# Performance work log

Hardware: AMD Instinct MI355X
Metric: run time of the kernel (lower is better)

Reference implementation:

```python
import jax, jax.numpy as jnp
import numpy as np

TEMPERATURE = 0.07
EPS = 1e-6  # arccosh domain clamp: argument must be >= 1


def setup_inputs() -> dict:
    key = jax.random.key(0)
    k1, k2 = jax.random.split(key)
    N, D = 8192, 768
    v_hyp = jax.random.normal(k1, (N, D), dtype=jnp.float32)
    t_hyp = jax.random.normal(k2, (N, D), dtype=jnp.float32)
    c = jnp.float32(1.0)  # curvature (positive scalar)
    return {"v_hyp": v_hyp, "t_hyp": t_hyp, "c": c}


def _pairwise_hyperbolic_dist(v, t, c):
    # Lorentz/hyperboloid pairwise distance with curvature c:
    #   x_time = sqrt(1/c + ||x||^2)
    #   <x,y>_L = x . y - x_time * y_time
    #   d(x,y) = (1/sqrt(c)) * arccosh(clamp(-c * <x,y>_L, min=1+eps))
    inv_c = 1.0 / c
    v_time = jnp.sqrt(inv_c + jnp.sum(v * v, axis=-1))  # [N]
    t_time = jnp.sqrt(inv_c + jnp.sum(t * t, axis=-1))  # [N]
    lorentz = jnp.einsum("nd,md->nm", v, t) - v_time[:, None] * t_time[None, :]
    arg = jnp.maximum(-c * lorentz, 1.0 + EPS)
    return jnp.sqrt(inv_c) * jnp.arccosh(arg)  # [N, N]


def _ce_diag(logits):
    # cross-entropy with labels = arange(N), mean reduction
    logp = jax.nn.log_softmax(logits, axis=-1)
    return -jnp.mean(jnp.diagonal(logp))


def reference(v_hyp, t_hyp, c):
    dist = _pairwise_hyperbolic_dist(v_hyp, t_hyp, c)
    logits = -dist / TEMPERATURE  # [N, N]
    loss_v2t = _ce_diag(logits)
    loss_t2v = _ce_diag(logits.T)
    return (loss_v2t + loss_t2v) * 0.5
```

## Files before the change

### kernel.cpp

```cpp
#include <hip/hip_runtime.h>
#include <hip/hip_bf16.h>
#include <math.h>

#define NROWS 8192
#define DDIM  768
#define TEMP_INV 14.285714285714286f
#define EPSX 1e-6f
#define NKT  12
#define SHIFT 55.0f
#define SHIFT_E 79.34282475f
#define QS   20.0f
#define SLOT 16384

typedef __attribute__((ext_vector_type(4))) int   i32x4;
typedef unsigned int   u32;

#define GLOAD16(gaddr, laddr)                                                   \
  __builtin_amdgcn_global_load_lds(                                             \
      (const __attribute__((address_space(1))) u32*)(gaddr),                    \
      (__attribute__((address_space(3))) u32*)(laddr), 16, 0, 0)

#define MFMAI8(a,b,c) __builtin_amdgcn_mfma_i32_16x16x64_i8((a),(b),(c),0,0,0)

__device__ __forceinline__ u32 q8(float x){
  int q = __float2int_rn(x * QS);
  q = q < -127 ? -127 : (q > 127 ? 127 : q);
  return (u32)(q & 255);
}

template<int CTRL>
__device__ __forceinline__ float dpp_rot_add(float v){
  int r = __builtin_amdgcn_update_dpp(0, __float_as_int(v), CTRL, 0xF, 0xF, true);
  return v + __int_as_float(r);
}
__device__ __forceinline__ float row_sum16(float v){
  v = dpp_rot_add<0x121>(v);
  v = dpp_rot_add<0x122>(v);
  v = dpp_rot_add<0x124>(v);
  v = dpp_rot_add<0x128>(v);
  return v;
}

__global__ __launch_bounds__(256) void prep_kernel(
    const float* __restrict__ v, const float* __restrict__ t, const float* __restrict__ cptr,
    u32* __restrict__ vb, u32* __restrict__ tb,
    float* __restrict__ vtime, float* __restrict__ ttime, float* __restrict__ diag)
{
  const int row  = blockIdx.x * 4 + (threadIdx.x >> 6);
  const int lane = threadIdx.x & 63;
  const float inv_c = 1.0f / cptr[0];
  const float4* vr = (const float4*)(v + (size_t)row * DDIM);
  const float4* tr = (const float4*)(t + (size_t)row * DDIM);
  u32* vbr = vb + (size_t)row * (DDIM/4);
  u32* tbr = tb + (size_t)row * (DDIM/4);
  float sv = 0.f, st = 0.f, dd = 0.f;
  #pragma unroll
  for (int it = 0; it < 3; it++){
    int k = lane + it*64;
    float4 a = vr[k], b = tr[k];
    sv += a.x*a.x + a.y*a.y + a.z*a.z + a.w*a.w;
    st += b.x*b.x + b.y*b.y + b.z*b.z + b.w*b.w;
    dd += a.x*b.x + a.y*b.y + a.z*b.z + a.w*b.w;
    vbr[k] = q8(a.x) | (q8(a.y)<<8) | (q8(a.z)<<16) | (q8(a.w)<<24);
    tbr[k] = q8(b.x) | (q8(b.y)<<8) | (q8(b.z)<<16) | (q8(b.w)<<24);
  }
  #pragma unroll
  for (int o = 32; o; o >>= 1){
    sv += __shfl_down(sv, o);
    st += __shfl_down(st, o);
    dd += __shfl_down(dd, o);
  }
  if (!lane){
    vtime[row] = sqrtf(inv_c + sv);
    ttime[row] = sqrtf(inv_c + st);
    diag[row]  = dd;
  }
}

__global__ __launch_bounds__(512, 6) void tile_kernel(
    const char* __restrict__ vb, const char* __restrict__ tb,
    const float* __restrict__ vtime, const float* __restrict__ ttime,
    const float* __restrict__ cptr,
    float* __restrict__ rowPsum, float* __restrict__ colPsum)
{
  __shared__ char SMc[3*SLOT];
  __shared__ float vtl2[128], ttl[128];

  const int tid = threadIdx.x;
  const int lane = tid & 63, wid = tid >> 6;
  const int wm = wid >> 1, wn = wid & 1;
  const int lo = lane & 15, hi = lane >> 4;

  const float c = cptr[0];
  const float c2 = c + c;
  const float slog = -(1.0f/sqrtf(c)) * TEMP_INV;
  const float wmin = c2 * (1.0f + EPSX);
  const float kq   = c2 * (1.0f/(QS*QS));

  const int linear = blockIdx.x;
  const int xcd = linear & 7, s = linear >> 3;
  const int xr = xcd & 1, xc = xcd >> 1;
  const int by = xr*32 + (s & 3) + ((s >> 6) << 2);
  const int bx = xc*16 + ((s >> 2) & 15);

  if (tid < 128){ vtl2[tid] = c2 * vtime[by*128 + tid]; }
  else if (tid < 256){ ttl[tid-128] = ttime[bx*128 + tid - 128]; }

  const char* Abase = vb + (size_t)(by*128) * DDIM;
  const char* Bbase = tb + (size_t)(bx*128) * DDIM;

  const int sx = (tid >> 3) & 3;
  const char* pA = Abase + (size_t)(tid >> 2)*DDIM + ((tid & 3) ^ sx)*16;
  const char* pB = Bbase + (size_t)(tid >> 2)*DDIM + ((tid & 3) ^ sx)*16;
  const int dA = wid*1024;
  const int dB = 8192 + wid*1024;

  const int swb  = (hi ^ ((lo >> 1) & 3)) * 16;
  const int arow = (wm*32 + lo) * 64 + swb;
  const int brow = 8192 + (wn*64 + lo) * 64 + swb;

  i32x4 acc[2][4];
  #pragma unroll
  for (int m = 0; m < 2; m++)
    #pragma unroll
    for (int n = 0; n < 4; n++)
      acc[m][n] = (i32x4){0,0,0,0};

#define STG(kt) do{                                                              \
    char* s_ = SMc + ((kt) % 3) * SLOT;                                          \
    GLOAD16(pA + (kt)*64, s_ + dA);                                              \
    GLOAD16(pB + (kt)*64, s_ + dB); }while(0)

  STG(0); STG(1);
  asm volatile("s_waitcnt vmcnt(2) lgkmcnt(0)" ::: "memory");
  __builtin_amdgcn_s_barrier();

  #pragma unroll
  for (int t = 0; t < NKT; t++){
    __builtin_amdgcn_sched_barrier(0);
    const char* S = SMc + (t % 3) * SLOT;
    if (t + 2 < NKT) STG(t + 2);
    i32x4 b[4];
    #pragma unroll
    for (int n = 0; n < 4; n++) b[n] = *(const i32x4*)(S + brow + n*1024);
    i32x4 a0 = *(const i32x4*)(S + arow);
    i32x4 a1 = *(const i32x4*)(S + arow + 1024);
    __builtin_amdgcn_s_setprio(1);
    #pragma unroll
    for (int n = 0; n < 4; n++){
      acc[0][n] = MFMAI8(a0, b[n], acc[0][n]);
      acc[1][n] = MFMAI8(a1, b[n], acc[1][n]);
    }
    __builtin_amdgcn_s_setprio(0);
    if (t < NKT-2)       asm volatile("s_waitcnt vmcnt(2) lgkmcnt(0)" ::: "memory");
    else if (t == NKT-2) asm volatile("s_waitcnt vmcnt(0) lgkmcnt(0)" ::: "memory");
    else                 asm volatile("s_waitcnt lgkmcnt(0)" ::: "memory");
    __builtin_amdgcn_s_barrier();
  }
#undef STG

  __syncthreads();

  #pragma unroll
  for (int m = 0; m < 2; m++){
    #pragma unroll
    for (int n = 0; n < 4; n++){
      #pragma unroll
      for (int q = 0; q < 4; q++){
        int r  = wm*32 + m*16 + hi*4 + q;
        int cc = wn*64 + n*16 + lo;
        float w = fmaf(-kq, (float)acc[m][n][q], vtl2[r] * ttl[cc]);
        w = fmaxf(w, wmin);
        acc[m][n][q] = __float_as_int(exp2f(fmaf(slog, log2f(w), SHIFT_E)));
      }
    }
  }

  float* reds  = (float*)SMc;
  float* redcs = reds + 256;

  #pragma unroll
  for (int m = 0; m < 2; m++){
    #pragma unroll
    for (int q = 0; q < 4; q++){
      float s2 = (__int_as_float(acc[m][0][q]) + __int_as_float(acc[m][1][q]))
               + (__int_as_float(acc[m][2][q]) + __int_as_float(acc[m][3][q]));
      s2 = row_sum16(s2);
      if (lo == 0)
        reds[wn*128 + wm*32 + m*16 + hi*4 + q] = s2;
    }
  }
  __syncthreads();
  if (tid < 128){
    float S = reds[tid] + reds[128 + tid];
    rowPsum[(size_t)bx*NROWS + by*128 + tid] = S;
  }

  #pragma unroll
  for (int n = 0; n < 4; n++){
    float s2 = 0.f;
    #pragma unroll
    for (int m = 0; m < 2; m++)
      #pragma unroll
      for (int q = 0; q < 4; q++) s2 += __int_as_float(acc[m][n][q]);
    s2 += __shfl_xor(s2, 16);
    s2 += __shfl_xor(s2, 32);
    if (hi == 0)
      redcs[wm*128 + wn*64 + n*16 + lo] = s2;
  }
  __syncthreads();
  if (tid < 128){
    float S = (redcs[tid] + redcs[128 + tid]) + (redcs[256 + tid] + redcs[384 + tid]);
    colPsum[(size_t)by*NROWS + bx*128 + tid] = S;
  }
}

__global__ __launch_bounds__(256) void lse_reduce(
    const float* __restrict__ rowPsum, const float* __restrict__ colPsum,
    float* __restrict__ psums)
{
  const int i = blockIdx.x * 256 + threadIdx.x;
  const float* Ps = blockIdx.y ? colPsum : rowPsum;
  float S = 0.f;
  for (int b = 0; b < 64; b++)
    S += Ps[(size_t)b*NROWS + i];
  float lse = __logf(S) - SHIFT;
  for (int o = 32; o; o >>= 1) lse += __shfl_down(lse, o);
  __shared__ float red[4];
  int lane = threadIdx.x & 63, wid = threadIdx.x >> 6;
  if (!lane) red[wid] = lse;
  __syncthreads();
  if (!threadIdx.x)
    psums[blockIdx.y*32 + blockIdx.x] = red[0]+red[1]+red[2]+red[3];
}

__global__ __launch_bounds__(1024) void final_kernel(
    const float* __restrict__ psums, const float* __restrict__ vtime,
    const float* __restrict__ ttime, const float* __restrict__ diag,
    const float* __restrict__ cptr, float* __restrict__ out)
{
  int tid = threadIdx.x;
  float c = cptr[0];
  float slog = -(1.0f/sqrtf(c)) * TEMP_INV;
  float dsum = 0.f;
  #pragma unroll
  for (int it = 0; it < 8; it++){
    int i = tid + it*1024;
    float arg = c * (vtime[i]*ttime[i] - diag[i]);
    arg = fmaxf(arg, 1.0f + EPSX);
    dsum += slog * __logf(arg + sqrtf(arg*arg - 1.0f));
  }
  for (int o = 32; o; o >>= 1) dsum += __shfl_down(dsum, o);
  __shared__ float red[16];
  if (!(tid & 63)) red[tid >> 6] = dsum;
  __syncthreads();
  if (tid < 64){
    float p = psums[tid];
    for (int o = 32; o; o >>= 1) p += __shfl_down(p, o);
    if (!tid){
      float dtot = 0.f;
      #pragma unroll
      for (int k = 0; k < 16; k++) dtot += red[k];
      out[0] = 0.5f*p/NROWS - dtot/NROWS;
    }
  }
}

extern "C" void kernel_launch(void* const* d_in, const int* in_sizes, int n_in,
                              void* d_out, int out_size, void* d_ws, size_t ws_size,
                              hipStream_t stream) {
  const float* v = (const float*)d_in[0];
  const float* t = (const float*)d_in[1];
  const float* c = (const float*)d_in[2];

  char* ws = (char*)d_ws;
  const size_t NB = (size_t)NROWS * DDIM;
  char*  vb      = ws;
  char*  tb      = ws + NB;
  float* vtime   = (float*)(ws + 2*NB);
  float* ttime   = (float*)(ws + 2*NB + NROWS*4);
  float* diag    = (float*)(ws + 2*NB + 2*(size_t)NROWS*4);
  char*  p       = ws + 2*NB + 3*(size_t)NROWS*4;
  float* rowPsum = (float*)(p);
  float* colPsum = (float*)(p + (size_t)64*NROWS*4);
  float* psums   = (float*)(p + (size_t)128*NROWS*4);

  prep_kernel<<<2048, 256, 0, stream>>>(v, t, c, (u32*)vb, (u32*)tb, vtime, ttime, diag);
  tile_kernel<<<4096, 512, 0, stream>>>(vb, tb, vtime, ttime, c, rowPsum, colPsum);
  lse_reduce<<<dim3(32, 2), 256, 0, stream>>>(rowPsum, colPsum, psums);
  final_kernel<<<1, 1024, 0, stream>>>(psums, vtime, ttime, diag, c, (float*)d_out);
}
```

Baseline: 101.4 us.

## Store quantized int8 operands in k-tile planar pre-swizzled layout

The prep kernel now writes the int8-quantized v and t matrices as 12 k-tile planes, each holding 64 bytes per row, with the LDS bank swizzle already applied. The tile kernel's async global-to-LDS loads therefore read one contiguous 1 KB chunk per wave per stage instead of 64-byte pieces strided by the row length. This should improve global-load coalescing and simplify address math in the GEMM loop. In exchange, the prep kernel uses only 48 of 64 lanes and writes 16-byte stores scattered across planes.

```diff
diff --git a/kernel.cpp b/kernel.cpp
--- a/kernel.cpp
+++ b/kernel.cpp
@@ -11,6 +11,7 @@
 #define SHIFT_E 79.34282475f
 #define QS   20.0f
 #define SLOT 16384
+#define PLANE ((size_t)NROWS * 64)
 
 typedef __attribute__((ext_vector_type(4))) int   i32x4;
 typedef unsigned int   u32;
@@ -43,7 +44,7 @@
 
 __global__ __launch_bounds__(256) void prep_kernel(
     const float* __restrict__ v, const float* __restrict__ t, const float* __restrict__ cptr,
-    u32* __restrict__ vb, u32* __restrict__ tb,
+    char* __restrict__ vp, char* __restrict__ tp,
     float* __restrict__ vtime, float* __restrict__ ttime, float* __restrict__ diag)
 {
   const int row  = blockIdx.x * 4 + (threadIdx.x >> 6);
@@ -51,18 +52,28 @@
   const float inv_c = 1.0f / cptr[0];
   const float4* vr = (const float4*)(v + (size_t)row * DDIM);
   const float4* tr = (const float4*)(t + (size_t)row * DDIM);
-  u32* vbr = vb + (size_t)row * (DDIM/4);
-  u32* tbr = tb + (size_t)row * (DDIM/4);
   float sv = 0.f, st = 0.f, dd = 0.f;
-  #pragma unroll
-  for (int it = 0; it < 3; it++){
-    int k = lane + it*64;
-    float4 a = vr[k], b = tr[k];
-    sv += a.x*a.x + a.y*a.y + a.z*a.z + a.w*a.w;
-    st += b.x*b.x + b.y*b.y + b.z*b.z + b.w*b.w;
-    dd += a.x*b.x + a.y*b.y + a.z*b.z + a.w*b.w;
-    vbr[k] = q8(a.x) | (q8(a.y)<<8) | (q8(a.z)<<16) | (q8(a.w)<<24);
-    tbr[k] = q8(b.x) | (q8(b.y)<<8) | (q8(b.z)<<16) | (q8(b.w)<<24);
+  if (lane < 48){
+    float4 va[4], ta[4];
+    #pragma unroll
+    for (int j = 0; j < 4; j++){ va[j] = vr[lane*4 + j]; ta[j] = tr[lane*4 + j]; }
+    #pragma unroll
+    for (int j = 0; j < 4; j++){
+      sv += va[j].x*va[j].x + va[j].y*va[j].y + va[j].z*va[j].z + va[j].w*va[j].w;
+      st += ta[j].x*ta[j].x + ta[j].y*ta[j].y + ta[j].z*ta[j].z + ta[j].w*ta[j].w;
+      dd += va[j].x*ta[j].x + va[j].y*ta[j].y + va[j].z*ta[j].z + va[j].w*ta[j].w;
+    }
+    i32x4 pv, pt;
+    #pragma unroll
+    for (int j = 0; j < 4; j++){
+      pv[j] = (int)(q8(va[j].x) | (q8(va[j].y)<<8) | (q8(va[j].z)<<16) | (q8(va[j].w)<<24));
+      pt[j] = (int)(q8(ta[j].x) | (q8(ta[j].y)<<8) | (q8(ta[j].z)<<16) | (q8(ta[j].w)<<24));
+    }
+    const int kt = lane >> 2;
+    const int c  = (lane & 3) ^ ((row >> 1) & 3);
+    const size_t off = (size_t)kt*PLANE + (size_t)row*64 + c*16;
+    *(i32x4*)(vp + off) = pv;
+    *(i32x4*)(tp + off) = pt;
   }
   #pragma unroll
   for (int o = 32; o; o >>= 1){
@@ -78,7 +89,7 @@
 }
 
 __global__ __launch_bounds__(512, 6) void tile_kernel(
-    const char* __restrict__ vb, const char* __restrict__ tb,
+    const char* __restrict__ vp, const char* __restrict__ tp,
     const float* __restrict__ vtime, const float* __restrict__ ttime,
     const float* __restrict__ cptr,
     float* __restrict__ rowPsum, float* __restrict__ colPsum)
@@ -106,12 +117,8 @@
   if (tid < 128){ vtl2[tid] = c2 * vtime[by*128 + tid]; }
   else if (tid < 256){ ttl[tid-128] = ttime[bx*128 + tid - 128]; }
 
-  const char* Abase = vb + (size_t)(by*128) * DDIM;
-  const char* Bbase = tb + (size_t)(bx*128) * DDIM;
-
-  const int sx = (tid >> 3) & 3;
-  const char* pA = Abase + (size_t)(tid >> 2)*DDIM + ((tid & 3) ^ sx)*16;
-  const char* pB = Bbase + (size_t)(tid >> 2)*DDIM + ((tid & 3) ^ sx)*16;
+  const char* pA0 = vp + ((size_t)(by*128 + (wid<<4)) << 6) + (lane << 4);
+  const char* pB0 = tp + ((size_t)(bx*128 + (wid<<4)) << 6) + (lane << 4);
   const int dA = wid*1024;
   const int dB = 8192 + wid*1024;
 
@@ -128,8 +135,8 @@
 
 #define STG(kt) do{                                                              \
     char* s_ = SMc + ((kt) % 3) * SLOT;                                          \
-    GLOAD16(pA + (kt)*64, s_ + dA);                                              \
-    GLOAD16(pB + (kt)*64, s_ + dB); }while(0)
+    GLOAD16(pA0 + (size_t)(kt)*PLANE, s_ + dA);                                  \
+    GLOAD16(pB0 + (size_t)(kt)*PLANE, s_ + dB); }while(0)
 
   STG(0); STG(1);
   asm volatile("s_waitcnt vmcnt(2) lgkmcnt(0)" ::: "memory");
@@ -275,8 +282,8 @@
 
   char* ws = (char*)d_ws;
   const size_t NB = (size_t)NROWS * DDIM;
-  char*  vb      = ws;
-  char*  tb      = ws + NB;
+  char*  vp      = ws;
+  char*  tp      = ws + NB;
   float* vtime   = (float*)(ws + 2*NB);
   float* ttime   = (float*)(ws + 2*NB + NROWS*4);
   float* diag    = (float*)(ws + 2*NB + 2*(size_t)NROWS*4);
@@ -285,8 +292,8 @@
   float* colPsum = (float*)(p + (size_t)64*NROWS*4);
   float* psums   = (float*)(p + (size_t)128*NROWS*4);
 
-  prep_kernel<<<2048, 256, 0, stream>>>(v, t, c, (u32*)vb, (u32*)tb, vtime, ttime, diag);
-  tile_kernel<<<4096, 512, 0, stream>>>(vb, tb, vtime, ttime, c, rowPsum, colPsum);
+  prep_kernel<<<2048, 256, 0, stream>>>(v, t, c, vp, tp, vtime, ttime, diag);
+  tile_kernel<<<4096, 512, 0, stream>>>(vp, tp, vtime, ttime, c, rowPsum, colPsum);
   lse_reduce<<<dim3(32, 2), 256, 0, stream>>>(rowPsum, colPsum, psums);
   final_kernel<<<1, 1024, 0, stream>>>(psums, vtime, ttime, diag, c, (float*)d_out);
 }
```

Measured after the change: 103.5 us. 2.0% more time.
